# Kernel tuning notes

Measured on AMD Instinct MI355X. Metric: run time of the kernel, lower is better.

The kernel has to match this reference:

```python
import jax
jax.config.update("jax_enable_x64", True)
import jax.numpy as jnp
import numpy as np

SCALE = 1 << 16  # 65536 fixed-point scale
HALF = SCALE // 2

DIM = 4096
HIDDEN = 11008  # multiple_of * ceil(int(2*16384/3)/256)
TOKENS = 1024


def setup_inputs() -> dict:
    key = jax.random.key(0)
    kx, k1, k2, k3 = jax.random.split(key, 4)
    # Integer-valued fixed-point activations (torch code treats x as int32).
    x = jax.random.randint(kx, (TOKENS, DIM), 0, 256, dtype=jnp.int32)
    # Learned float weights (quantized to int32 fixed-point inside forward).
    w1 = jax.random.normal(k1, (HIDDEN, DIM), dtype=jnp.float32) * 0.02
    w2 = jax.random.normal(k2, (DIM, HIDDEN), dtype=jnp.float32) * 0.02
    w3 = jax.random.normal(k3, (HIDDEN, DIM), dtype=jnp.float32) * 0.02
    return {"x": x, "w1": w1, "w2": w2, "w3": w3}


def reference(x, w1, w2, w3):
    # Quantize weights to int32 fixed point (round half-to-even, like torch.round).
    w1i = jnp.round(w1.astype(jnp.float64) * SCALE).astype(jnp.int32)
    w2i = jnp.round(w2.astype(jnp.float64) * SCALE).astype(jnp.int32)
    w3i = jnp.round(w3.astype(jnp.float64) * SCALE).astype(jnp.int32)

    xf = x.astype(jnp.float64)  # [T, D]
    # Emulated integer GEMMs via fp64 matmul, truncated to int64 (exact here).
    t1 = jnp.matmul(xf, w1i.T.astype(jnp.float64)).astype(jnp.int64)  # [T, H]
    t3 = jnp.matmul(xf, w3i.T.astype(jnp.float64)).astype(jnp.int64)  # [T, H]

    # Requantize up-projection: rounding floor-div by SCALE (int floor division).
    q3 = ((t3 + HALF) // SCALE).astype(jnp.int32)

    # Gate path: requantize, dequantize to fp16, SiLU, re-quantize to int32.
    g = (t1 + HALF) // SCALE
    g = (g.astype(jnp.float64) / SCALE).astype(jnp.float16)
    g = jax.nn.silu(g)  # fp16 SiLU, matching F.silu on half
    g = jnp.round(g.astype(jnp.float64) * SCALE).astype(jnp.int32)

    # Fixed-point elementwise product with rounding requantization.
    t13 = ((g.astype(jnp.int64) * q3.astype(jnp.int64) + HALF) // SCALE).astype(jnp.int32)

    # Down projection GEMM + final requantization.
    t123 = jnp.matmul(t13.astype(jnp.float64), w2i.T.astype(jnp.float64)).astype(jnp.int64)
    out = ((t123 + HALF) // SCALE).astype(jnp.int32)  # [T, D]
    return out
```

## Files before the change

### kernel.cpp

```cpp
#include <hip/hip_runtime.h>
#include <hip/hip_fp16.h>
#include <math.h>

#define TOK  1024
#define DIMK 4096
#define HID  11008

typedef long long ll;
typedef int v4i  __attribute__((ext_vector_type(4)));
typedef int v16i __attribute__((ext_vector_type(16)));

#define T13_OFF 0ull
#define LUT_OFF 11272192ull
#define CS1_OFF (LUT_OFF + 32768ull)
#define CS3_OFF (CS1_OFF + 44032ull)
#define XQ_OFF  (CS3_OFF + 44032ull)
#define WQ_OFF  (XQ_OFF + 4194304ull)
#define PLANE   45088768ull
#define WS_NEED (WQ_OFF + 6ull * PLANE)

__device__ __forceinline__ int gate_requant(int g) {
  const float vf = __half2float(__float2half((float)g * (1.0f / 65536.0f)));
  const float e32 = (float)exp(-(double)vf);
  const float e16 = __half2float(__float2half(e32));
  const float d16 = __half2float(__float2half(1.0f + e16));
  const float s16 = __half2float(__float2half(1.0f / d16));
  const float p16 = __half2float(__float2half(vf * s16));
  return __float2int_rn(p16 * 65536.0f);
}

__device__ __forceinline__ v16i vzero16() {
  v16i z;
  #pragma unroll
  for (int i = 0; i < 16; ++i) z[i] = 0;
  return z;
}

__device__ __forceinline__ void gll(const void* g, void* l) {
  __builtin_amdgcn_global_load_lds((const __attribute__((address_space(1))) unsigned int*)g,
                                   (__attribute__((address_space(3))) unsigned int*)l,
                                   16, 0, 0);
}


__global__ void lut_kernel(int* __restrict__ lut) {
  const int i = blockIdx.x * blockDim.x + threadIdx.x;
  lut[i] = gate_requant(i - 4096);
}

__global__ __launch_bounds__(256)
void xq_kernel(const int* __restrict__ x, char* __restrict__ xq) {
  const size_t base = ((size_t)blockIdx.x * 256 + threadIdx.x) * 16;
  int w[4];
  #pragma unroll
  for (int i = 0; i < 4; ++i) {
    const int4 v = *reinterpret_cast<const int4*>(&x[base + i * 4]);
    w[i] = ((v.x & 255) | ((v.y & 255) << 8) | ((v.z & 255) << 16) | ((v.w & 255) << 24)) ^ 0x80808080;
  }
  *reinterpret_cast<int4*>(&xq[base]) = make_int4(w[0], w[1], w[2], w[3]);
}

__global__ __launch_bounds__(256)
void prequant_all(const float* __restrict__ w1, const float* __restrict__ w3,
                  const float* __restrict__ w2, char* __restrict__ wq,
                  int* __restrict__ cs1, int* __restrict__ cs3)
{
  const int bid = blockIdx.x;
  const int m = bid / 11008;
  const int rb = bid - m * 11008;
  const float* src = (m == 0) ? w1 : ((m == 1) ? w3 : w2);
  int* lo = (int*)(wq + (size_t)(2 * m) * PLANE);
  int* hi = (int*)(wq + (size_t)(2 * m + 1) * PLANE);
  const size_t f4base = (size_t)rb * 1024;

  int sum = 0;
  #pragma unroll
  for (int j = 0; j < 4; ++j) {
    const size_t f4 = f4base + threadIdx.x + j * 256;
    const float4 f = *reinterpret_cast<const float4*>(&src[f4 * 4]);
    const int q0 = __float2int_rn(f.x * 65536.0f);
    const int q1 = __float2int_rn(f.y * 65536.0f);
    const int q2 = __float2int_rn(f.z * 65536.0f);
    const int q3 = __float2int_rn(f.w * 65536.0f);
    sum += q0 + q1 + q2 + q3;
    lo[f4] = (q0 & 127) | ((q1 & 127) << 8) | ((q2 & 127) << 16) | ((q3 & 127) << 24);
    hi[f4] = ((q0 >> 7) & 255) | (((q1 >> 7) & 255) << 8) |
             (((q2 >> 7) & 255) << 16) | (((q3 >> 7) & 255) << 24);
  }
  if (m < 2) {
    #pragma unroll
    for (int off = 32; off > 0; off >>= 1) sum += __shfl_xor(sum, off, 64);
    if ((threadIdx.x & 63) == 0) atomicAdd(((m == 0) ? cs1 : cs3) + rb, sum);
  }
}

#define UP_BUF 32768

__global__ __launch_bounds__(512, 1)
void up_gemm(const char* __restrict__ xq, const char* __restrict__ wq,
             const int* __restrict__ csum1, const int* __restrict__ csum3,
             const int* __restrict__ lut, char* __restrict__ t13)
{
  __shared__ char smem[3 * UP_BUF];
  const int tid = threadIdx.x;
  const int w = tid >> 6, l = tid & 63;
  const int rf = w & 3, cf = w >> 2;
  const int l16 = l * 16;

  const int flat = blockIdx.x;
  const int g = (flat & 7) * 86 + (flat >> 3);
  const int col0 = (g >> 2) * 64;
  const int row0 = (g & 3) * 256;

  const char* gA = xq + (size_t)(row0 + w * 32 + (l & 31)) * DIMK + (l >> 5) * 16;
  const char* gB = wq + (size_t)(w >> 1) * PLANE
                 + (size_t)(col0 + (w & 1) * 32 + (l & 31)) * DIMK + (l >> 5) * 16;
  const unsigned dA0 = (2 * w + 0) * 1024, dA1 = (2 * w + 1) * 1024;
  const unsigned dB0 = 16384 + (2 * w + 0) * 1024, dB1 = 16384 + (2 * w + 1) * 1024;

  v16i acc[2][4];
  #pragma unroll
  for (int m = 0; m < 2; ++m)
    #pragma unroll
    for (int p = 0; p < 4; ++p) acc[m][p] = vzero16();

  #define UP_STAGE(kb, bo) { \
    gll(gA + (kb), smem + (bo) + dA0);      gll(gA + (kb) + 32, smem + (bo) + dA1); \
    gll(gB + (kb), smem + (bo) + dB0);      gll(gB + (kb) + 32, smem + (bo) + dB1); }

  #define UP_PHASE(ks) { \
    const v4i av0 = *(const v4i*)(sb + (rf * 4 + 0 + (ks)) * 1024 + l16); \
    const v4i av1 = *(const v4i*)(sb + (rf * 4 + 2 + (ks)) * 1024 + l16); \
    const v4i b0  = *(const v4i*)(sb + 16384 + (0 * 4 + cf * 2 + (ks)) * 1024 + l16); \
    const v4i b1  = *(const v4i*)(sb + 16384 + (1 * 4 + cf * 2 + (ks)) * 1024 + l16); \
    const v4i b2  = *(const v4i*)(sb + 16384 + (2 * 4 + cf * 2 + (ks)) * 1024 + l16); \
    const v4i b3  = *(const v4i*)(sb + 16384 + (3 * 4 + cf * 2 + (ks)) * 1024 + l16); \
    __builtin_amdgcn_s_setprio(1); \
    acc[0][0] = __builtin_amdgcn_mfma_i32_32x32x32_i8(av0, b0, acc[0][0], 0, 0, 0); \
    acc[0][1] = __builtin_amdgcn_mfma_i32_32x32x32_i8(av0, b1, acc[0][1], 0, 0, 0); \
    acc[0][2] = __builtin_amdgcn_mfma_i32_32x32x32_i8(av0, b2, acc[0][2], 0, 0, 0); \
    acc[0][3] = __builtin_amdgcn_mfma_i32_32x32x32_i8(av0, b3, acc[0][3], 0, 0, 0); \
    acc[1][0] = __builtin_amdgcn_mfma_i32_32x32x32_i8(av1, b0, acc[1][0], 0, 0, 0); \
    acc[1][1] = __builtin_amdgcn_mfma_i32_32x32x32_i8(av1, b1, acc[1][1], 0, 0, 0); \
    acc[1][2] = __builtin_amdgcn_mfma_i32_32x32x32_i8(av1, b2, acc[1][2], 0, 0, 0); \
    acc[1][3] = __builtin_amdgcn_mfma_i32_32x32x32_i8(av1, b3, acc[1][3], 0, 0, 0); \
    __builtin_amdgcn_s_setprio(0); }

  UP_STAGE(0, 0);
  UP_STAGE(64, UP_BUF);

  const int NT = DIMK / 64;
  unsigned co = 0, so = 2 * UP_BUF;
  for (int kt = 0; kt < NT; ++kt) {
    if (kt + 2 < NT) {
      UP_STAGE((kt + 2) * 64, so);
      so = (so == 2 * UP_BUF) ? 0 : so + UP_BUF;
      asm volatile("s_waitcnt vmcnt(8)" ::: "memory");
    } else if (kt + 1 < NT) {
      asm volatile("s_waitcnt vmcnt(4)" ::: "memory");
    } else {
      asm volatile("s_waitcnt vmcnt(0)" ::: "memory");
    }
    __builtin_amdgcn_s_barrier();
    const char* sb = smem + co;
    UP_PHASE(0)
    UP_PHASE(1)
    __builtin_amdgcn_s_barrier();
    co = (co == 2 * UP_BUF) ? 0 : co + UP_BUF;
  }
  #undef UP_STAGE
  #undef UP_PHASE

  const int col = col0 + cf * 32 + (l & 31);
  const int cs1v = csum1[col], cs3v = csum3[col];
  #pragma unroll
  for (int m = 0; m < 2; ++m) {
    #pragma unroll
    for (int r = 0; r < 16; ++r) {
      const int row = row0 + rf * 64 + m * 32 + (r & 3) + 8 * (r >> 2) + 4 * (l >> 5);
      const ll t1 = (ll)acc[m][0][r] + (((ll)acc[m][1][r] + cs1v) << 7);
      int gg = (int)((t1 + 32768) >> 16);
      gg = gg < -4096 ? -4096 : (gg > 4095 ? 4095 : gg);
      const ll t3 = (ll)acc[m][2][r] + (((ll)acc[m][3][r] + cs3v) << 7);
      const int q3 = (int)((t3 + 32768) >> 16);
      const int gate = lut[gg + 4096];
      t13[(size_t)row * HID + col] = (char)((int)(((ll)gate * q3 + 32768) >> 16));
    }
  }
}

#define DN_BUF 24576

__global__ __launch_bounds__(512, 1)
void down_gemm(const char* __restrict__ t13, const char* __restrict__ w2lo,
               const char* __restrict__ w2hi, int* __restrict__ out)
{
  __shared__ char smem[3 * DN_BUF];
  const int tid = threadIdx.x;
  const int w = tid >> 6, l = tid & 63;
  const int rf = w & 3, cf = w >> 2;
  const int l16 = l * 16;

  const int flat = blockIdx.x;
  const int g = (flat & 7) * 32 + (flat >> 3);
  const int col0 = (g >> 2) * 64;
  const int row0 = (g & 3) * 256;

  const char* gA = t13 + (size_t)(row0 + w * 32 + (l & 31)) * HID + (l >> 5) * 16;
  const char* pB = (w >> 2) ? w2hi : w2lo;
  const char* gB = pB + (size_t)(col0 + ((w >> 1) & 1) * 32 + (l & 31)) * HID
                 + (w & 1) * 32 + (l >> 5) * 16;
  const unsigned dA0 = (2 * w + 0) * 1024, dA1 = (2 * w + 1) * 1024;
  const unsigned dB = 16384 + w * 1024;

  v16i acc[2][2];
  #pragma unroll
  for (int m = 0; m < 2; ++m)
    #pragma unroll
    for (int p = 0; p < 2; ++p) acc[m][p] = vzero16();

  #define DN_STAGE(kb, bo) { \
    gll(gA + (kb), smem + (bo) + dA0);  gll(gA + (kb) + 32, smem + (bo) + dA1); \
    gll(gB + (kb), smem + (bo) + dB); }

  #define DN_PHASE(ks) { \
    const v4i av0 = *(const v4i*)(sb + (rf * 4 + 0 + (ks)) * 1024 + l16); \
    const v4i av1 = *(const v4i*)(sb + (rf * 4 + 2 + (ks)) * 1024 + l16); \
    const v4i bL  = *(const v4i*)(sb + 16384 + (0 * 4 + cf * 2 + (ks)) * 1024 + l16); \
    const v4i bH  = *(const v4i*)(sb + 16384 + (1 * 4 + cf * 2 + (ks)) * 1024 + l16); \
    __builtin_amdgcn_s_setprio(1); \
    acc[0][0] = __builtin_amdgcn_mfma_i32_32x32x32_i8(av0, bL, acc[0][0], 0, 0, 0); \
    acc[0][1] = __builtin_amdgcn_mfma_i32_32x32x32_i8(av0, bH, acc[0][1], 0, 0, 0); \
    acc[1][0] = __builtin_amdgcn_mfma_i32_32x32x32_i8(av1, bL, acc[1][0], 0, 0, 0); \
    acc[1][1] = __builtin_amdgcn_mfma_i32_32x32x32_i8(av1, bH, acc[1][1], 0, 0, 0); \
    __builtin_amdgcn_s_setprio(0); }

  DN_STAGE(0, 0);
  DN_STAGE(64, DN_BUF);

  const int NT = HID / 64;
  unsigned co = 0, so = 2 * DN_BUF;
  for (int kt = 0; kt < NT; ++kt) {
    if (kt + 2 < NT) {
      DN_STAGE((kt + 2) * 64, so);
      so = (so == 2 * DN_BUF) ? 0 : so + DN_BUF;
      asm volatile("s_waitcnt vmcnt(6)" ::: "memory");
    } else if (kt + 1 < NT) {
      asm volatile("s_waitcnt vmcnt(3)" ::: "memory");
    } else {
      asm volatile("s_waitcnt vmcnt(0)" ::: "memory");
    }
    __builtin_amdgcn_s_barrier();
    const char* sb = smem + co;
    DN_PHASE(0)
    DN_PHASE(1)
    __builtin_amdgcn_s_barrier();
    co = (co == 2 * DN_BUF) ? 0 : co + DN_BUF;
  }
  #undef DN_STAGE
  #undef DN_PHASE

  const int col = col0 + cf * 32 + (l & 31);
  #pragma unroll
  for (int m = 0; m < 2; ++m) {
    #pragma unroll
    for (int r = 0; r < 16; ++r) {
      const int row = row0 + rf * 64 + m * 32 + (r & 3) + 8 * (r >> 2) + 4 * (l >> 5);
      out[(size_t)row * DIMK + col] =
          (int)((((ll)acc[m][0][r] + ((ll)acc[m][1][r] << 7)) + 32768) >> 16);
    }
  }
}

#define BT 64
#define BN 64
#define BK 64
#define LDST 68

__device__ __forceinline__ int mad24(int a, int b, int c) {
  return ((a << 8) >> 8) * ((b << 8) >> 8) + c;
}

__global__ __launch_bounds__(256)
void ffn_up_f(const int* __restrict__ x, const float* __restrict__ w1,
              const float* __restrict__ w3, short* __restrict__ t13)
{
  __shared__ int As[BT][LDST];
  __shared__ int B1[BK][LDST];
  __shared__ int B3[BK][LDST];
  const int tx = threadIdx.x, ty = threadIdx.y;
  const int tid = ty * 16 + tx;
  const int col0 = blockIdx.x * BN;
  const int row0 = blockIdx.y * BT;
  const int lr = tid >> 4;
  const int lk = (tid & 15) << 2;
  int acc1[16] = {0};
  int acc3[16] = {0};
  for (int k0 = 0; k0 < DIMK; k0 += BK) {
    #pragma unroll
    for (int m = 0; m < 4; ++m) {
      const int r = lr + m * 16;
      *reinterpret_cast<int4*>(&As[r][lk]) =
          *reinterpret_cast<const int4*>(&x[(size_t)(row0 + r) * DIMK + k0 + lk]);
      const float4 f1 = *reinterpret_cast<const float4*>(&w1[(size_t)(col0 + r) * DIMK + k0 + lk]);
      const float4 f3 = *reinterpret_cast<const float4*>(&w3[(size_t)(col0 + r) * DIMK + k0 + lk]);
      B1[lk + 0][r] = __float2int_rn(f1.x * 65536.0f);
      B1[lk + 1][r] = __float2int_rn(f1.y * 65536.0f);
      B1[lk + 2][r] = __float2int_rn(f1.z * 65536.0f);
      B1[lk + 3][r] = __float2int_rn(f1.w * 65536.0f);
      B3[lk + 0][r] = __float2int_rn(f3.x * 65536.0f);
      B3[lk + 1][r] = __float2int_rn(f3.y * 65536.0f);
      B3[lk + 2][r] = __float2int_rn(f3.z * 65536.0f);
      B3[lk + 3][r] = __float2int_rn(f3.w * 65536.0f);
    }
    __syncthreads();
    #pragma unroll 8
    for (int kk = 0; kk < BK; ++kk) {
      const int4 b1 = *reinterpret_cast<const int4*>(&B1[kk][tx << 2]);
      const int4 b3 = *reinterpret_cast<const int4*>(&B3[kk][tx << 2]);
      #pragma unroll
      for (int i = 0; i < 4; ++i) {
        const int av = As[(ty << 2) + i][kk] & 255;
        acc1[i*4+0] = mad24(av, b1.x, acc1[i*4+0]);
        acc1[i*4+1] = mad24(av, b1.y, acc1[i*4+1]);
        acc1[i*4+2] = mad24(av, b1.z, acc1[i*4+2]);
        acc1[i*4+3] = mad24(av, b1.w, acc1[i*4+3]);
        acc3[i*4+0] = mad24(av, b3.x, acc3[i*4+0]);
        acc3[i*4+1] = mad24(av, b3.y, acc3[i*4+1]);
        acc3[i*4+2] = mad24(av, b3.z, acc3[i*4+2]);
        acc3[i*4+3] = mad24(av, b3.w, acc3[i*4+3]);
      }
    }
    __syncthreads();
  }
  #pragma unroll
  for (int i = 0; i < 4; ++i) {
    #pragma unroll
    for (int j = 0; j < 4; ++j) {
      const int g    = (acc1[i*4+j] + 32768) >> 16;
      const int q3   = (acc3[i*4+j] + 32768) >> 16;
      const int gate = gate_requant(g);
      const int tv = (int)(((ll)gate * (ll)q3 + 32768) >> 16);
      t13[(size_t)(row0 + (ty<<2) + i) * HID + col0 + (tx<<2) + j] = (short)tv;
    }
  }
}

__global__ __launch_bounds__(256)
void ffn_down_f(const short* __restrict__ t13, const float* __restrict__ w2,
                int* __restrict__ out)
{
  __shared__ int As[BT][LDST];
  __shared__ int Bs[BK][LDST];
  const int tx = threadIdx.x, ty = threadIdx.y;
  const int tid = ty * 16 + tx;
  const int col0 = blockIdx.x * BN;
  const int row0 = blockIdx.y * BT;
  const int lr = tid >> 4;
  const int lk = (tid & 15) << 2;
  const int ar = tid >> 3;
  const int ak = (tid & 7) << 3;
  int acc[16] = {0};
  for (int k0 = 0; k0 < HID; k0 += BK) {
    #pragma unroll
    for (int m = 0; m < 2; ++m) {
      const int r = ar + m * 32;
      const int4 v = *reinterpret_cast<const int4*>(&t13[(size_t)(row0 + r) * HID + k0 + ak]);
      As[r][ak+0] = (v.x << 16) >> 16;  As[r][ak+1] = v.x >> 16;
      As[r][ak+2] = (v.y << 16) >> 16;  As[r][ak+3] = v.y >> 16;
      As[r][ak+4] = (v.z << 16) >> 16;  As[r][ak+5] = v.z >> 16;
      As[r][ak+6] = (v.w << 16) >> 16;  As[r][ak+7] = v.w >> 16;
    }
    #pragma unroll
    for (int m = 0; m < 4; ++m) {
      const int r = lr + m * 16;
      const float4 f = *reinterpret_cast<const float4*>(&w2[(size_t)(col0 + r) * HID + k0 + lk]);
      Bs[lk + 0][r] = __float2int_rn(f.x * 65536.0f);
      Bs[lk + 1][r] = __float2int_rn(f.y * 65536.0f);
      Bs[lk + 2][r] = __float2int_rn(f.z * 65536.0f);
      Bs[lk + 3][r] = __float2int_rn(f.w * 65536.0f);
    }
    __syncthreads();
    #pragma unroll 8
    for (int kk = 0; kk < BK; ++kk) {
      const int4 b = *reinterpret_cast<const int4*>(&Bs[kk][tx << 2]);
      #pragma unroll
      for (int i = 0; i < 4; ++i) {
        const int av = As[(ty << 2) + i][kk];
        acc[i*4+0] = mad24(av, b.x, acc[i*4+0]);
        acc[i*4+1] = mad24(av, b.y, acc[i*4+1]);
        acc[i*4+2] = mad24(av, b.z, acc[i*4+2]);
        acc[i*4+3] = mad24(av, b.w, acc[i*4+3]);
      }
    }
    __syncthreads();
  }
  #pragma unroll
  for (int i = 0; i < 4; ++i) {
    #pragma unroll
    for (int j = 0; j < 4; ++j) {
      out[(size_t)(row0 + (ty<<2) + i) * DIMK + col0 + (tx<<2) + j] =
          (acc[i*4+j] + 32768) >> 16;
    }
  }
}

extern "C" void kernel_launch(void* const* d_in, const int* in_sizes, int n_in,
                              void* d_out, int out_size, void* d_ws, size_t ws_size,
                              hipStream_t stream) {
  (void)in_sizes; (void)n_in; (void)out_size;
  const int*   x  = (const int*)d_in[0];
  const float* w1 = (const float*)d_in[1];
  const float* w2 = (const float*)d_in[2];
  const float* w3 = (const float*)d_in[3];
  int* out = (int*)d_out;
  char* ws = (char*)d_ws;

  if (ws_size >= WS_NEED) {
    char* t13 = ws + T13_OFF;
    int*  lut = (int*)(ws + LUT_OFF);
    int*  cs1 = (int*)(ws + CS1_OFF);
    int*  cs3 = (int*)(ws + CS3_OFF);
    char* xq  = ws + XQ_OFF;
    char* wq  = ws + WQ_OFF;

    hipMemsetAsync(ws + CS1_OFF, 0, 88064, stream);
    hipLaunchKernelGGL(lut_kernel, dim3(32), dim3(256), 0, stream, lut);
    hipLaunchKernelGGL(xq_kernel, dim3(1024), dim3(256), 0, stream, x, xq);
    hipLaunchKernelGGL(prequant_all, dim3(33024), dim3(256), 0, stream,
                       w1, w3, w2, wq, cs1, cs3);
    hipLaunchKernelGGL(up_gemm, dim3(688), dim3(512), 0, stream,
                       xq, wq, cs1, cs3, lut, t13);
    hipLaunchKernelGGL(down_gemm, dim3(256), dim3(512), 0, stream,
                       t13, wq + 4 * PLANE, wq + 5 * PLANE, out);
  } else {
    if (ws_size < (size_t)TOK * HID * sizeof(short)) return;
    short* t13 = (short*)ws;
    dim3 blk(16, 16);
    hipLaunchKernelGGL(ffn_up_f,   dim3(HID / BN, TOK / BT), blk, 0, stream, x, w1, w3, t13);
    hipLaunchKernelGGL(ffn_down_f, dim3(DIMK / BN, TOK / BT), blk, 0, stream, t13, w2, out);
  }
}
```

Baseline: 578.1 us.

## Interleave global-to-LDS loads with MFMA phases using ping-pong barriers

Restructures the main loops of both the up- and down-projection int8 GEMMs. The A and B global-to-LDS loads for tile kt+2 are now issued inside separate half-phases, each followed by a barrier, with MFMA bursts fenced by sched_barrier. The vmcnt wait moves to the end of each iteration. The aim is a wavefront ping-pong schedule where memory issue and MFMA work alternate across waves, hiding load latency better. It adds an extra barrier per iteration and depends on the reworked waitcnt accounting being correct.

```diff
diff --git a/kernel.cpp b/kernel.cpp
--- a/kernel.cpp
+++ b/kernel.cpp
@@ -124,52 +124,70 @@
     #pragma unroll
     for (int p = 0; p < 4; ++p) acc[m][p] = vzero16();
 
-  #define UP_STAGE(kb, bo) { \
-    gll(gA + (kb), smem + (bo) + dA0);      gll(gA + (kb) + 32, smem + (bo) + dA1); \
-    gll(gB + (kb), smem + (bo) + dB0);      gll(gB + (kb) + 32, smem + (bo) + dB1); }
-
-  #define UP_PHASE(ks) { \
-    const v4i av0 = *(const v4i*)(sb + (rf * 4 + 0 + (ks)) * 1024 + l16); \
-    const v4i av1 = *(const v4i*)(sb + (rf * 4 + 2 + (ks)) * 1024 + l16); \
-    const v4i b0  = *(const v4i*)(sb + 16384 + (0 * 4 + cf * 2 + (ks)) * 1024 + l16); \
-    const v4i b1  = *(const v4i*)(sb + 16384 + (1 * 4 + cf * 2 + (ks)) * 1024 + l16); \
-    const v4i b2  = *(const v4i*)(sb + 16384 + (2 * 4 + cf * 2 + (ks)) * 1024 + l16); \
-    const v4i b3  = *(const v4i*)(sb + 16384 + (3 * 4 + cf * 2 + (ks)) * 1024 + l16); \
-    __builtin_amdgcn_s_setprio(1); \
-    acc[0][0] = __builtin_amdgcn_mfma_i32_32x32x32_i8(av0, b0, acc[0][0], 0, 0, 0); \
-    acc[0][1] = __builtin_amdgcn_mfma_i32_32x32x32_i8(av0, b1, acc[0][1], 0, 0, 0); \
-    acc[0][2] = __builtin_amdgcn_mfma_i32_32x32x32_i8(av0, b2, acc[0][2], 0, 0, 0); \
-    acc[0][3] = __builtin_amdgcn_mfma_i32_32x32x32_i8(av0, b3, acc[0][3], 0, 0, 0); \
-    acc[1][0] = __builtin_amdgcn_mfma_i32_32x32x32_i8(av1, b0, acc[1][0], 0, 0, 0); \
-    acc[1][1] = __builtin_amdgcn_mfma_i32_32x32x32_i8(av1, b1, acc[1][1], 0, 0, 0); \
-    acc[1][2] = __builtin_amdgcn_mfma_i32_32x32x32_i8(av1, b2, acc[1][2], 0, 0, 0); \
-    acc[1][3] = __builtin_amdgcn_mfma_i32_32x32x32_i8(av1, b3, acc[1][3], 0, 0, 0); \
-    __builtin_amdgcn_s_setprio(0); }
-
-  UP_STAGE(0, 0);
-  UP_STAGE(64, UP_BUF);
+  gll(gA, smem + dA0);       gll(gA + 32, smem + dA1);
+  gll(gB, smem + dB0);       gll(gB + 32, smem + dB1);
+  gll(gA + 64, smem + UP_BUF + dA0);  gll(gA + 96, smem + UP_BUF + dA1);
+  gll(gB + 64, smem + UP_BUF + dB0);  gll(gB + 96, smem + UP_BUF + dB1);
+  asm volatile("s_waitcnt vmcnt(4)" ::: "memory");
+  __builtin_amdgcn_s_barrier();
 
   const int NT = DIMK / 64;
   unsigned co = 0, so = 2 * UP_BUF;
   for (int kt = 0; kt < NT; ++kt) {
-    if (kt + 2 < NT) {
-      UP_STAGE((kt + 2) * 64, so);
-      so = (so == 2 * UP_BUF) ? 0 : so + UP_BUF;
-      asm volatile("s_waitcnt vmcnt(8)" ::: "memory");
-    } else if (kt + 1 < NT) {
-      asm volatile("s_waitcnt vmcnt(4)" ::: "memory");
-    } else {
-      asm volatile("s_waitcnt vmcnt(0)" ::: "memory");
-    }
-    __builtin_amdgcn_s_barrier();
     const char* sb = smem + co;
-    UP_PHASE(0)
-    UP_PHASE(1)
-    __builtin_amdgcn_s_barrier();
+    const bool st = (kt + 2 < NT);
+    const int kb = (kt + 2) * 64;
+    {
+      const v4i av0 = *(const v4i*)(sb + (rf * 4 + 0) * 1024 + l16);
+      const v4i av1 = *(const v4i*)(sb + (rf * 4 + 2) * 1024 + l16);
+      const v4i b0  = *(const v4i*)(sb + 16384 + (0 * 4 + cf * 2) * 1024 + l16);
+      const v4i b1  = *(const v4i*)(sb + 16384 + (1 * 4 + cf * 2) * 1024 + l16);
+      const v4i b2  = *(const v4i*)(sb + 16384 + (2 * 4 + cf * 2) * 1024 + l16);
+      const v4i b3  = *(const v4i*)(sb + 16384 + (3 * 4 + cf * 2) * 1024 + l16);
+      if (st) { gll(gA + kb, smem + so + dA0); gll(gA + kb + 32, smem + so + dA1); }
+      __builtin_amdgcn_s_barrier();
+      asm volatile("s_waitcnt lgkmcnt(0)" ::: "memory");
+      __builtin_amdgcn_sched_barrier(0);
+      __builtin_amdgcn_s_setprio(1);
+      acc[0][0] = __builtin_amdgcn_mfma_i32_32x32x32_i8(av0, b0, acc[0][0], 0, 0, 0);
+      acc[0][1] = __builtin_amdgcn_mfma_i32_32x32x32_i8(av0, b1, acc[0][1], 0, 0, 0);
+      acc[0][2] = __builtin_amdgcn_mfma_i32_32x32x32_i8(av0, b2, acc[0][2], 0, 0, 0);
+      acc[0][3] = __builtin_amdgcn_mfma_i32_32x32x32_i8(av0, b3, acc[0][3], 0, 0, 0);
+      acc[1][0] = __builtin_amdgcn_mfma_i32_32x32x32_i8(av1, b0, acc[1][0], 0, 0, 0);
+      acc[1][1] = __builtin_amdgcn_mfma_i32_32x32x32_i8(av1, b1, acc[1][1], 0, 0, 0);
+      acc[1][2] = __builtin_amdgcn_mfma_i32_32x32x32_i8(av1, b2, acc[1][2], 0, 0, 0);
+      acc[1][3] = __builtin_amdgcn_mfma_i32_32x32x32_i8(av1, b3, acc[1][3], 0, 0, 0);
+      __builtin_amdgcn_s_setprio(0);
+      __builtin_amdgcn_s_barrier();
+    }
+    {
+      const v4i av0 = *(const v4i*)(sb + (rf * 4 + 1) * 1024 + l16);
+      const v4i av1 = *(const v4i*)(sb + (rf * 4 + 3) * 1024 + l16);
+      const v4i b0  = *(const v4i*)(sb + 16384 + (0 * 4 + cf * 2 + 1) * 1024 + l16);
+      const v4i b1  = *(const v4i*)(sb + 16384 + (1 * 4 + cf * 2 + 1) * 1024 + l16);
+      const v4i b2  = *(const v4i*)(sb + 16384 + (2 * 4 + cf * 2 + 1) * 1024 + l16);
+      const v4i b3  = *(const v4i*)(sb + 16384 + (3 * 4 + cf * 2 + 1) * 1024 + l16);
+      if (st) { gll(gB + kb, smem + so + dB0); gll(gB + kb + 32, smem + so + dB1); }
+      __builtin_amdgcn_s_barrier();
+      asm volatile("s_waitcnt lgkmcnt(0)" ::: "memory");
+      __builtin_amdgcn_sched_barrier(0);
+      __builtin_amdgcn_s_setprio(1);
+      acc[0][0] = __builtin_amdgcn_mfma_i32_32x32x32_i8(av0, b0, acc[0][0], 0, 0, 0);
+      acc[0][1] = __builtin_amdgcn_mfma_i32_32x32x32_i8(av0, b1, acc[0][1], 0, 0, 0);
+      acc[0][2] = __builtin_amdgcn_mfma_i32_32x32x32_i8(av0, b2, acc[0][2], 0, 0, 0);
+      acc[0][3] = __builtin_amdgcn_mfma_i32_32x32x32_i8(av0, b3, acc[0][3], 0, 0, 0);
+      acc[1][0] = __builtin_amdgcn_mfma_i32_32x32x32_i8(av1, b0, acc[1][0], 0, 0, 0);
+      acc[1][1] = __builtin_amdgcn_mfma_i32_32x32x32_i8(av1, b1, acc[1][1], 0, 0, 0);
+      acc[1][2] = __builtin_amdgcn_mfma_i32_32x32x32_i8(av1, b2, acc[1][2], 0, 0, 0);
+      acc[1][3] = __builtin_amdgcn_mfma_i32_32x32x32_i8(av1, b3, acc[1][3], 0, 0, 0);
+      __builtin_amdgcn_s_setprio(0);
+      if (st) { asm volatile("s_waitcnt vmcnt(4)" ::: "memory"); }
+      else    { asm volatile("s_waitcnt vmcnt(0)" ::: "memory"); }
+      __builtin_amdgcn_s_barrier();
+    }
+    if (st) so = (so == 2 * UP_BUF) ? 0 : so + UP_BUF;
     co = (co == 2 * UP_BUF) ? 0 : co + UP_BUF;
   }
-  #undef UP_STAGE
-  #undef UP_PHASE
 
   const int col = col0 + cf * 32 + (l & 31);
   const int cs1v = csum1[col], cs3v = csum3[col];
@@ -219,46 +237,57 @@
     #pragma unroll
     for (int p = 0; p < 2; ++p) acc[m][p] = vzero16();
 
-  #define DN_STAGE(kb, bo) { \
-    gll(gA + (kb), smem + (bo) + dA0);  gll(gA + (kb) + 32, smem + (bo) + dA1); \
-    gll(gB + (kb), smem + (bo) + dB); }
-
-  #define DN_PHASE(ks) { \
-    const v4i av0 = *(const v4i*)(sb + (rf * 4 + 0 + (ks)) * 1024 + l16); \
-    const v4i av1 = *(const v4i*)(sb + (rf * 4 + 2 + (ks)) * 1024 + l16); \
-    const v4i bL  = *(const v4i*)(sb + 16384 + (0 * 4 + cf * 2 + (ks)) * 1024 + l16); \
-    const v4i bH  = *(const v4i*)(sb + 16384 + (1 * 4 + cf * 2 + (ks)) * 1024 + l16); \
-    __builtin_amdgcn_s_setprio(1); \
-    acc[0][0] = __builtin_amdgcn_mfma_i32_32x32x32_i8(av0, bL, acc[0][0], 0, 0, 0); \
-    acc[0][1] = __builtin_amdgcn_mfma_i32_32x32x32_i8(av0, bH, acc[0][1], 0, 0, 0); \
-    acc[1][0] = __builtin_amdgcn_mfma_i32_32x32x32_i8(av1, bL, acc[1][0], 0, 0, 0); \
-    acc[1][1] = __builtin_amdgcn_mfma_i32_32x32x32_i8(av1, bH, acc[1][1], 0, 0, 0); \
-    __builtin_amdgcn_s_setprio(0); }
-
-  DN_STAGE(0, 0);
-  DN_STAGE(64, DN_BUF);
+  gll(gA, smem + dA0);  gll(gA + 32, smem + dA1);  gll(gB, smem + dB);
+  gll(gA + 64, smem + DN_BUF + dA0);  gll(gA + 96, smem + DN_BUF + dA1);
+  gll(gB + 64, smem + DN_BUF + dB);
+  asm volatile("s_waitcnt vmcnt(3)" ::: "memory");
+  __builtin_amdgcn_s_barrier();
 
   const int NT = HID / 64;
   unsigned co = 0, so = 2 * DN_BUF;
   for (int kt = 0; kt < NT; ++kt) {
-    if (kt + 2 < NT) {
-      DN_STAGE((kt + 2) * 64, so);
-      so = (so == 2 * DN_BUF) ? 0 : so + DN_BUF;
-      asm volatile("s_waitcnt vmcnt(6)" ::: "memory");
-    } else if (kt + 1 < NT) {
-      asm volatile("s_waitcnt vmcnt(3)" ::: "memory");
-    } else {
-      asm volatile("s_waitcnt vmcnt(0)" ::: "memory");
-    }
-    __builtin_amdgcn_s_barrier();
     const char* sb = smem + co;
-    DN_PHASE(0)
-    DN_PHASE(1)
-    __builtin_amdgcn_s_barrier();
+    const bool st = (kt + 2 < NT);
+    const int kb = (kt + 2) * 64;
+    {
+      const v4i av0 = *(const v4i*)(sb + (rf * 4 + 0) * 1024 + l16);
+      const v4i av1 = *(const v4i*)(sb + (rf * 4 + 2) * 1024 + l16);
+      const v4i bL  = *(const v4i*)(sb + 16384 + (0 * 4 + cf * 2) * 1024 + l16);
+      const v4i bH  = *(const v4i*)(sb + 16384 + (1 * 4 + cf * 2) * 1024 + l16);
+      if (st) { gll(gA + kb, smem + so + dA0); gll(gA + kb + 32, smem + so + dA1); }
+      __builtin_amdgcn_s_barrier();
+      asm volatile("s_waitcnt lgkmcnt(0)" ::: "memory");
+      __builtin_amdgcn_sched_barrier(0);
+      __builtin_amdgcn_s_setprio(1);
+      acc[0][0] = __builtin_amdgcn_mfma_i32_32x32x32_i8(av0, bL, acc[0][0], 0, 0, 0);
+      acc[0][1] = __builtin_amdgcn_mfma_i32_32x32x32_i8(av0, bH, acc[0][1], 0, 0, 0);
+      acc[1][0] = __builtin_amdgcn_mfma_i32_32x32x32_i8(av1, bL, acc[1][0], 0, 0, 0);
+      acc[1][1] = __builtin_amdgcn_mfma_i32_32x32x32_i8(av1, bH, acc[1][1], 0, 0, 0);
+      __builtin_amdgcn_s_setprio(0);
+      __builtin_amdgcn_s_barrier();
+    }
+    {
+      const v4i av0 = *(const v4i*)(sb + (rf * 4 + 1) * 1024 + l16);
+      const v4i av1 = *(const v4i*)(sb + (rf * 4 + 3) * 1024 + l16);
+      const v4i bL  = *(const v4i*)(sb + 16384 + (0 * 4 + cf * 2 + 1) * 1024 + l16);
+      const v4i bH  = *(const v4i*)(sb + 16384 + (1 * 4 + cf * 2 + 1) * 1024 + l16);
+      if (st) { gll(gB + kb, smem + so + dB); }
+      __builtin_amdgcn_s_barrier();
+      asm volatile("s_waitcnt lgkmcnt(0)" ::: "memory");
+      __builtin_amdgcn_sched_barrier(0);
+      __builtin_amdgcn_s_setprio(1);
+      acc[0][0] = __builtin_amdgcn_mfma_i32_32x32x32_i8(av0, bL, acc[0][0], 0, 0, 0);
+      acc[0][1] = __builtin_amdgcn_mfma_i32_32x32x32_i8(av0, bH, acc[0][1], 0, 0, 0);
+      acc[1][0] = __builtin_amdgcn_mfma_i32_32x32x32_i8(av1, bL, acc[1][0], 0, 0, 0);
+      acc[1][1] = __builtin_amdgcn_mfma_i32_32x32x32_i8(av1, bH, acc[1][1], 0, 0, 0);
+      __builtin_amdgcn_s_setprio(0);
+      if (st) { asm volatile("s_waitcnt vmcnt(3)" ::: "memory"); }
+      else    { asm volatile("s_waitcnt vmcnt(0)" ::: "memory"); }
+      __builtin_amdgcn_s_barrier();
+    }
+    if (st) so = (so == 2 * DN_BUF) ? 0 : so + DN_BUF;
     co = (co == 2 * DN_BUF) ? 0 : co + DN_BUF;
   }
-  #undef DN_STAGE
-  #undef DN_PHASE
 
   const int col = col0 + cf * 32 + (l & 31);
   #pragma unroll
```

Measured after the change: 515.5 us. 1.12x faster.
